# Kernel optimization log

Measured on AMD Instinct MI355X. Metric: run time of the kernel, lower is better.

## Reference

```python
import jax, jax.numpy as jnp
import numpy as np

H = 2048        # hidden_size
NH = 16         # num_heads
NOPE = 128      # qk_nope_head_dim
ROPE = 64       # qk_rope_head_dim
VD = 128        # v_head_dim
QLORA = 1536    # q_lora_rank
KVLORA = 512    # kv_lora_rank
THETA = 1000000.0
EPS = 1e-6
B, S = 2, 2048


def _rope_cos_sin(position_ids):
    # inv_freq over even dims, emb = cat(freqs, freqs); indexed by position_ids
    inv_freq = 1.0 / (THETA ** (jnp.arange(0, ROPE, 2, dtype=jnp.float32) / ROPE))
    freqs = position_ids.astype(jnp.float32)[..., None] * inv_freq  # [b,s,ROPE/2]
    emb = jnp.concatenate([freqs, freqs], axis=-1)                  # [b,s,ROPE]
    # unsqueeze_dim=1 -> broadcast over heads
    return jnp.cos(emb)[:, None], jnp.sin(emb)[:, None]             # [b,1,s,ROPE]


def _apply_rope(x, cos, sin):
    # torch: view(b,h,s,d//2,2).transpose(4,3).reshape -> interleaved-to-half-split permutation
    xp = jnp.concatenate([x[..., 0::2], x[..., 1::2]], axis=-1)
    x1, x2 = jnp.split(xp, 2, axis=-1)
    rot = jnp.concatenate([-x2, x1], axis=-1)  # rotate_half
    return xp * cos + rot * sin


def setup_inputs() -> dict:
    key = jax.random.key(0)
    ks = jax.random.split(key, 7)
    s = 0.02
    hidden_states = jax.random.normal(ks[0], (B, S, H), jnp.float32)
    position_ids = jnp.broadcast_to(jnp.arange(S, dtype=jnp.int64 if jax.config.jax_enable_x64 else jnp.int32), (B, S))
    attention_mask = jnp.broadcast_to(jnp.tril(jnp.ones((S, S), bool))[None, None], (B, 1, S, S))
    Wq_down = jax.random.normal(ks[1], (QLORA, H), jnp.float32) * s
    q_ln_w = jnp.ones((QLORA,), jnp.float32)
    Wq_up = jax.random.normal(ks[2], (NH * (NOPE + ROPE), QLORA), jnp.float32) * s
    Wkv_down = jax.random.normal(ks[3], (KVLORA + ROPE, H), jnp.float32) * s
    Wkv_up = jax.random.normal(ks[4], (NH * (NOPE + VD), KVLORA), jnp.float32) * s
    Wo = jax.random.normal(ks[5], (H, NH * VD), jnp.float32) * s
    return {
        'hidden_states': hidden_states, 'position_ids': position_ids,
        'attention_mask': attention_mask, 'Wq_down': Wq_down, 'q_ln_w': q_ln_w,
        'Wq_up': Wq_up, 'Wkv_down': Wkv_down, 'Wkv_up': Wkv_up, 'Wo': Wo,
    }


def reference(hidden_states, position_ids, attention_mask,
              Wq_down, q_ln_w, Wq_up, Wkv_down, Wkv_up, Wo):
    b, s, _ = hidden_states.shape
    dtype = hidden_states.dtype

    # --- Q path: down-proj -> RMSNorm -> up-proj ---
    ql = hidden_states @ Wq_down.T                                   # [b,s,QLORA]
    var = jnp.mean(jnp.square(ql.astype(jnp.float32)), -1, keepdims=True)
    ql = (q_ln_w * (ql.astype(jnp.float32) * jax.lax.rsqrt(var + EPS)).astype(dtype))
    q = (ql @ Wq_up.T).reshape(b, s, NH, NOPE + ROPE).transpose(0, 2, 1, 3)  # [b,h,s,d]
    q_nope, q_rope = q[..., :NOPE], q[..., NOPE:]

    cos, sin = _rope_cos_sin(position_ids)                           # [b,1,s,ROPE]
    q_rope = _apply_rope(q_rope, cos, sin)                           # [b,h,s,ROPE]

    # --- KV path: single down-proj, split into compressed_kv and rope part ---
    ckv = hidden_states @ Wkv_down.T                                 # [b,s,KVLORA+ROPE]
    compressed_kv, k_rope = ckv[..., :KVLORA], ckv[..., KVLORA:]
    k_rope = _apply_rope(k_rope[:, None], cos, sin)[:, 0]            # [b,s,ROPE]
    # NOTE: kv_down_layernorm is declared in __init__ but never applied in forward.

    # --- absorption trick: fold kv_up into q / output ---
    kv_up = Wkv_up.reshape(NH, NOPE + VD, KVLORA)
    q_absorb = kv_up[:, :NOPE, :]                                    # [h,NOPE,KVLORA]
    out_absorb = kv_up[:, NOPE:, :]                                  # [h,VD,KVLORA]
    q_abs = jnp.einsum('bhsn,hnc->bhsc', q_nope, q_absorb)           # [b,h,s,KVLORA]

    scale = 1.0 / np.sqrt(NOPE + ROPE)
    scores = (jnp.einsum('bhqr,bkr->bhqk', q_rope, k_rope)
              + jnp.einsum('bhqc,bkc->bhqk', q_abs, compressed_kv)) * scale
    scores = jnp.where(attention_mask, scores, -jnp.inf)
    attn = jax.nn.softmax(scores.astype(jnp.float32), axis=-1).astype(dtype)

    out = jnp.einsum('bhqk,bkc->bhqc', attn, compressed_kv)          # [b,h,s,KVLORA]
    out = jnp.einsum('bhqc,hvc->bhqv', out, out_absorb)              # [b,h,s,VD]
    out = out.transpose(0, 2, 1, 3).reshape(b, s, NH * VD)
    return out @ Wo.T                                                # [b,s,H]
```

## Files before the change

kernel.cpp:

```cpp
#include <hip/hip_runtime.h>
#include <cstdint>

#define S_LEN 2048
#define NH_N  16
#define VT_LD 2080

typedef short s16x8 __attribute__((ext_vector_type(8)));
typedef unsigned short u16x8 __attribute__((ext_vector_type(8)));
typedef float f32x4 __attribute__((ext_vector_type(4)));

__device__ __forceinline__ float b2f(unsigned short u) {
    return __uint_as_float(((uint32_t)u) << 16);
}
__device__ __forceinline__ unsigned short f2b(float f) {
    uint32_t x = __float_as_uint(f);
    x += 0x7fffu + ((x >> 16) & 1u);
    return (unsigned short)(x >> 16);
}

__device__ __forceinline__ void cstore(unsigned short* p, float v) { *p = f2b(v); }
__device__ __forceinline__ void cstore(float* p, float v) { *p = v; }

__device__ __forceinline__ void gl2lds16(const void* g, void* l) {
    __builtin_amdgcn_global_load_lds(
        (const __attribute__((address_space(1))) unsigned int*)g,
        (__attribute__((address_space(3))) unsigned int*)l, 16, 0, 0);
}

__device__ __forceinline__ void lds_barrier() {
    asm volatile("s_waitcnt lgkmcnt(0)" ::: "memory");
    __builtin_amdgcn_s_barrier();
    __builtin_amdgcn_sched_barrier(0);
}

__global__ __launch_bounds__(256) void f32_to_bf16(const float* __restrict__ in,
                                                   unsigned short* __restrict__ out,
                                                   long n)
{
    const long nv = n >> 2;
    long i = (long)blockIdx.x * blockDim.x + threadIdx.x;
    const long stride = (long)gridDim.x * blockDim.x;
    for (; i < nv; i += stride) {
        float4 v = ((const float4*)in)[i];
        ushort4 o;
        o.x = f2b(v.x); o.y = f2b(v.y); o.z = f2b(v.z); o.w = f2b(v.w);
        ((ushort4*)out)[i] = o;
    }
}

template <typename CT>
__global__ __launch_bounds__(256) void gemm128(
    const unsigned short* __restrict__ A, const unsigned short* __restrict__ B,
    CT* __restrict__ C,
    int K, int lda, int ldb, int ldc, int Nlim,
    long sAb, long sAh, long sBb, long sBh, long sCb, long sCh)
{
    __shared__ unsigned short Alds[128 * 32];
    __shared__ unsigned short Blds[128 * 32];
    const int z = blockIdx.z, b = z >> 4, h = z & 15;
    A += (long)b * sAb + (long)h * sAh;
    B += (long)b * sBb + (long)h * sBh;
    C += (long)b * sCb + (long)h * sCh;
    const int tid = threadIdx.x;
    const int lane = tid & 63, w = tid >> 6;
    const int l15 = lane & 15, q4 = lane >> 4;
    const int m0 = blockIdx.x * 128, n0 = blockIdx.y * 128;
    const int wm = (w >> 1) * 64, wn = (w & 1) * 64;

    int srow[2], sgc[2];
#pragma unroll
    for (int it = 0; it < 2; ++it) {
        const int g = it * 256 + tid;
        const int row = g >> 2, gp = g & 3;
        srow[it] = row;
        sgc[it] = gp ^ ((row ^ (row >> 2)) & 3);
    }
    int aoff[4], boff[4];
#pragma unroll
    for (int i = 0; i < 4; ++i) {
        const int ra = wm + i * 16 + l15;
        aoff[i] = ra * 32 + (q4 ^ ((ra ^ (ra >> 2)) & 3)) * 8;
        const int rb = wn + i * 16 + l15;
        boff[i] = rb * 32 + (q4 ^ ((rb ^ (rb >> 2)) & 3)) * 8;
    }

    f32x4 acc[4][4];
#pragma unroll
    for (int i = 0; i < 4; ++i)
#pragma unroll
        for (int j = 0; j < 4; ++j) acc[i][j] = (f32x4){0.f, 0.f, 0.f, 0.f};

    for (int k0 = 0; k0 < K; k0 += 32) {
        __syncthreads();
#pragma unroll
        for (int it = 0; it < 2; ++it) {
            gl2lds16(A + (long)(m0 + srow[it]) * lda + k0 + sgc[it] * 8,
                     (char*)Alds + ((it * 256 + w * 64) << 4));
            gl2lds16(B + (long)(n0 + srow[it]) * ldb + k0 + sgc[it] * 8,
                     (char*)Blds + ((it * 256 + w * 64) << 4));
        }
        __syncthreads();
        s16x8 af[4], bf[4];
#pragma unroll
        for (int i = 0; i < 4; ++i) {
            af[i] = *(const s16x8*)(Alds + aoff[i]);
            bf[i] = *(const s16x8*)(Blds + boff[i]);
        }
#pragma unroll
        for (int i = 0; i < 4; ++i)
#pragma unroll
            for (int j = 0; j < 4; ++j)
                acc[i][j] = __builtin_amdgcn_mfma_f32_16x16x32_bf16(af[i], bf[j], acc[i][j], 0, 0, 0);
    }

#pragma unroll
    for (int i = 0; i < 4; ++i) {
        const int row0 = m0 + wm + i * 16 + q4 * 4;
#pragma unroll
        for (int j = 0; j < 4; ++j) {
            const int col = n0 + wn + j * 16 + l15;
            if (col < Nlim) {
#pragma unroll
                for (int r = 0; r < 4; ++r)
                    cstore(&C[(long)(row0 + r) * ldc + col], acc[i][j][r]);
            }
        }
    }
}

__global__ __launch_bounds__(256) void rmsnorm_k(unsigned short* __restrict__ ql,
                                                 const unsigned short* __restrict__ w)
{
    const long base = (long)blockIdx.x * 1536;
    const int tid = threadIdx.x;
    float v[6];
    float ss = 0.f;
#pragma unroll
    for (int i = 0; i < 6; ++i) {
        v[i] = b2f(ql[base + tid + i * 256]);
        ss += v[i] * v[i];
    }
#pragma unroll
    for (int off = 32; off; off >>= 1) ss += __shfl_xor(ss, off, 64);
    __shared__ float red[4];
    if ((tid & 63) == 0) red[tid >> 6] = ss;
    __syncthreads();
    const float tot = red[0] + red[1] + red[2] + red[3];
    const float r = rsqrtf(tot * (1.0f / 1536.0f) + 1e-6f);
#pragma unroll
    for (int i = 0; i < 6; ++i) {
        const int idx = tid + i * 256;
        ql[base + idx] = f2b(v[i] * r * b2f(w[idx]));
    }
}

__global__ __launch_bounds__(512) void rope_k(
    const unsigned short* __restrict__ q, const unsigned short* __restrict__ ckv,
    const int* __restrict__ pos_ids,
    unsigned short* __restrict__ q_rope, unsigned short* __restrict__ krope)
{
    const int bs = blockIdx.x;
    const int b = bs >> 11, s = bs & 2047;
    const int t = threadIdx.x;
    const int j = t & 31, h = t >> 5;
    const float pos = (float)pos_ids[bs];
    const float invf = __expf(-(float)j * 0.4317347f);
    float sn, cs;
    sincosf(pos * invf, &sn, &cs);
    const unsigned short* x = q + (long)bs * 3072 + h * 192 + 128;
    const float x0 = b2f(x[2 * j]), x1 = b2f(x[2 * j + 1]);
    const long ob = ((long)(b * NH_N + h) * S_LEN + s) * 64;
    q_rope[ob + j]      = f2b(x0 * cs - x1 * sn);
    q_rope[ob + 32 + j] = f2b(x1 * cs + x0 * sn);
    if (h == 0) {
        const unsigned short* y = ckv + (long)bs * 576 + 512;
        const float y0 = b2f(y[2 * j]), y1 = b2f(y[2 * j + 1]);
        const long ob2 = (long)bs * 64;
        krope[ob2 + j]      = f2b(y0 * cs - y1 * sn);
        krope[ob2 + 32 + j] = f2b(y1 * cs + y0 * sn);
    }
}

__global__ __launch_bounds__(256) void transpose_qabsorb(
    const unsigned short* __restrict__ Wkv_up, unsigned short* __restrict__ qT)
{
    const int idx = blockIdx.x * 256 + threadIdx.x;
    const int n = idx & 127;
    const int c = (idx >> 7) & 511;
    const int h = idx >> 16;
    qT[idx] = Wkv_up[((long)(h * 256 + n)) * 512 + c];
}

__global__ __launch_bounds__(256) void transpose_ckv(
    const unsigned short* __restrict__ ckv, unsigned short* __restrict__ VT_g)
{
    __shared__ unsigned short t[64][72];
    const int k0 = blockIdx.x * 64, c0 = blockIdx.y * 64, b = blockIdx.z;
    const int tid = threadIdx.x;
#pragma unroll
    for (int it = 0; it < 2; ++it) {
        int idx = tid + it * 256;
        int row = idx >> 3, g = idx & 7;
        *(s16x8*)&t[row][g * 8] =
            *(const s16x8*)(ckv + ((long)(b * S_LEN + k0 + row) * 576 + c0 + g * 8));
    }
    __syncthreads();
#pragma unroll
    for (int it = 0; it < 2; ++it) {
        int idx = tid + it * 256;
        int c = idx >> 3, g = idx & 7;
        u16x8 v;
#pragma unroll
        for (int j = 0; j < 8; ++j) v[j] = t[g * 8 + j][c];
        *(u16x8*)(VT_g + ((long)(b * 512 + c0 + c) * VT_LD + k0 + g * 8)) = v;
    }
}

__global__ __launch_bounds__(512, 1) void flash_mfma(
    const unsigned short* __restrict__ qabs,  const unsigned short* __restrict__ qrope,
    const unsigned short* __restrict__ ckv,   const unsigned short* __restrict__ krope,
    const unsigned short* __restrict__ VT_g,  unsigned short* __restrict__ attn_out)
{
    __shared__ unsigned short K_lds[2][2304 * 8];
    __shared__ unsigned short VT_lds[2][2048 * 8];
    __shared__ unsigned short P_lds[8][16 * 40];
    __shared__ float alpha_lds[8 * 16];
    __shared__ float inv_lds[8 * 16];
    __shared__ int   flag_lds[8];

    const float scale2 = 0.10412195f;
    const float THR    = 11.5416f;
    const int tid = threadIdx.x;
    const int lane = tid & 63, w = tid >> 6;
    const int l15 = lane & 15, q4 = lane >> 4;
    const int bh = blockIdx.x;
    const int b = bh >> 4;

    const unsigned short* ckv_b  = ckv   + (long)b * S_LEN * 576;
    const unsigned short* krop_b = krope + (long)b * S_LEN * 64;
    const unsigned short* vt_b   = VT_g  + (long)b * 512 * VT_LD;

    int koff[4], voff[4];
#pragma unroll
    for (int it = 0; it < 4; ++it) {
        const int idx = it * 512 + tid;
        const int key = ((idx >> 6) & 1) * 16 + (idx & 15);
        const int g   = (idx >> 7) * 4 + ((idx >> 4) & 3);
        koff[it] = key * 576 + g * 8;
        const int c   = (idx >> 6) * 16 + (idx & 15);
        voff[it] = c * VT_LD + ((idx >> 4) & 3) * 8;
    }
    const int hoff = (((tid >> 6) & 1) * 16 + (tid & 15)) * 64 +
                     ((tid >> 7) * 4 + ((tid >> 4) & 3)) * 8;

#pragma unroll 1
    for (int half = 0; half < 2; ++half) {
        const int qt = half ? blockIdx.y : 15 - blockIdx.y;
        const int q0 = qt * 128;

        s16x8 qf[18];
        {
            const unsigned short* qa = qabs + ((long)bh * S_LEN + q0 + w * 16 + l15) * 512 + q4 * 8;
#pragma unroll
            for (int kb = 0; kb < 16; ++kb) qf[kb] = *(const s16x8*)(qa + kb * 32);
            const unsigned short* qr = qrope + ((long)bh * S_LEN + q0 + w * 16 + l15) * 64 + q4 * 8;
            qf[16] = *(const s16x8*)(qr);
            qf[17] = *(const s16x8*)(qr + 32);
        }

        f32x4 O[32];
#pragma unroll
        for (int i = 0; i < 32; ++i) O[i] = (f32x4){0.f, 0.f, 0.f, 0.f};
        float m_i[4] = {-INFINITY, -INFINITY, -INFINITY, -INFINITY};
        float l_i[4] = {0.f, 0.f, 0.f, 0.f};

        const int nkt = 4 * qt + 4;
        unsigned short *Kc = K_lds[0], *Kn = K_lds[1];
        unsigned short *Vc = VT_lds[0], *Vn = VT_lds[1];

        {
#pragma unroll
            for (int it = 0; it < 4; ++it)
                gl2lds16(ckv_b + koff[it], (char*)Kc + ((it * 512 + w * 64) << 4));
            if (tid < 256)
                gl2lds16(krop_b + hoff, (char*)Kc + ((2048 + w * 64) << 4));
#pragma unroll
            for (int it = 0; it < 4; ++it)
                gl2lds16(vt_b + voff[it], (char*)Vc + ((it * 512 + w * 64) << 4));
        }
        __syncthreads();

        for (int kt = 0; kt < nkt; ++kt) {
            const int k0 = kt * 32;

            if (kt + 1 < nkt) {
                const int kn = k0 + 32;
                const unsigned short* cs = ckv_b + (long)kn * 576;
#pragma unroll
                for (int it = 0; it < 4; ++it)
                    gl2lds16(cs + koff[it], (char*)Kn + ((it * 512 + w * 64) << 4));
                if (tid < 256)
                    gl2lds16(krop_b + (long)kn * 64 + hoff, (char*)Kn + ((2048 + w * 64) << 4));
                const unsigned short* vs = vt_b + kn;
#pragma unroll
                for (int it = 0; it < 4; ++it)
                    gl2lds16(vs + voff[it], (char*)Vn + ((it * 512 + w * 64) << 4));
            }

            if (k0 <= q0 + (w << 4) + 15) {
                f32x4 s0 = {0.f, 0.f, 0.f, 0.f}, s1 = s0;
                __builtin_amdgcn_s_setprio(1);
#pragma unroll
                for (int kb = 0; kb < 18; ++kb) {
                    s16x8 k0f = *(const s16x8*)&Kc[((kb * 2 + 0) * 64 + lane) * 8];
                    s16x8 k1f = *(const s16x8*)&Kc[((kb * 2 + 1) * 64 + lane) * 8];
                    s0 = __builtin_amdgcn_mfma_f32_16x16x32_bf16(qf[kb], k0f, s0, 0, 0, 0);
                    s1 = __builtin_amdgcn_mfma_f32_16x16x32_bf16(qf[kb], k1f, s1, 0, 0, 0);
                }
                __builtin_amdgcn_s_setprio(0);
#pragma unroll
                for (int r = 0; r < 4; ++r) { s0[r] *= scale2; s1[r] *= scale2; }
                if (k0 + 31 > q0 + (w << 4)) {
#pragma unroll
                    for (int r = 0; r < 4; ++r) {
                        const int qg = q0 + w * 16 + q4 * 4 + r;
                        if (k0 + l15 > qg)      s0[r] = -INFINITY;
                        if (k0 + 16 + l15 > qg) s1[r] = -INFINITY;
                    }
                }

                float mx[4];
#pragma unroll
                for (int r = 0; r < 4; ++r) {
                    float m = fmaxf(s0[r], s1[r]);
#pragma unroll
                    for (int off = 1; off < 16; off <<= 1) m = fmaxf(m, __shfl_xor(m, off, 64));
                    mx[r] = m;
                }
                bool need = false;
#pragma unroll
                for (int r = 0; r < 4; ++r) need = need || (mx[r] - m_i[r] > THR);
                const bool needw = __any(need);
                float al[4] = {1.f, 1.f, 1.f, 1.f};
                if (needw) {
#pragma unroll
                    for (int r = 0; r < 4; ++r) {
                        const float mn = fmaxf(m_i[r], mx[r]);
                        al[r] = exp2f(m_i[r] - mn);
                        m_i[r] = mn;
                        l_i[r] *= al[r];
                    }
                }
                if (l15 == 0)
                    *(f32x4*)&alpha_lds[w * 16 + q4 * 4] = (f32x4){al[0], al[1], al[2], al[3]};
                if (lane == 0) flag_lds[w] = needw ? 1 : 0;
#pragma unroll
                for (int r = 0; r < 4; ++r) {
                    const float p0 = exp2f(s0[r] - m_i[r]);
                    const float p1 = exp2f(s1[r] - m_i[r]);
                    l_i[r] += p0 + p1;
                    P_lds[w][(q4 * 4 + r) * 40 + l15]      = f2b(p0);
                    P_lds[w][(q4 * 4 + r) * 40 + 16 + l15] = f2b(p1);
                }
            } else {
                if (lane == 0) flag_lds[w] = 0;
            }

            lds_barrier();

            {
                int4 f0 = *(const int4*)&flag_lds[0];
                int4 f1 = *(const int4*)&flag_lds[4];
                if (f0.x | f0.y | f0.z | f0.w | f1.x | f1.y | f1.z | f1.w) {
#pragma unroll
                    for (int rb = 0; rb < 8; ++rb) {
                        if (k0 <= q0 + rb * 16 + 15) {
                            f32x4 alr = *(const f32x4*)&alpha_lds[rb * 16 + q4 * 4];
#pragma unroll
                            for (int cb = 0; cb < 4; ++cb)
#pragma unroll
                                for (int r = 0; r < 4; ++r)
                                    O[rb * 4 + cb][r] *= alr[r];
                        }
                    }
                }
            }

            {
                s16x8 vh[4];
#pragma unroll
                for (int cb = 0; cb < 4; ++cb)
                    vh[cb] = *(const s16x8*)&Vc[((w * 4 + cb) * 64 + lane) * 8];
#pragma unroll
                for (int rb = 0; rb < 8; ++rb) {
                    if (k0 <= q0 + rb * 16 + 15) {
                        s16x8 pa = *(const s16x8*)&P_lds[rb][l15 * 40 + q4 * 8];
                        __builtin_amdgcn_s_setprio(1);
#pragma unroll
                        for (int cb = 0; cb < 4; ++cb)
                            O[rb * 4 + cb] = __builtin_amdgcn_mfma_f32_16x16x32_bf16(pa, vh[cb], O[rb * 4 + cb], 0, 0, 0);
                        __builtin_amdgcn_s_setprio(0);
                    }
                }
            }

            __syncthreads();
            unsigned short* t;
            t = Kc; Kc = Kn; Kn = t;
            t = Vc; Vc = Vn; Vn = t;
        }

#pragma unroll
        for (int r = 0; r < 4; ++r) {
            float ls = l_i[r];
#pragma unroll
            for (int off = 1; off < 16; off <<= 1) ls += __shfl_xor(ls, off, 64);
            l_i[r] = 1.0f / ls;
        }
        if (l15 == 0)
            *(f32x4*)&inv_lds[w * 16 + q4 * 4] = (f32x4){l_i[0], l_i[1], l_i[2], l_i[3]};
        lds_barrier();
#pragma unroll
        for (int rb = 0; rb < 8; ++rb) {
            f32x4 ivr = *(const f32x4*)&inv_lds[rb * 16 + q4 * 4];
#pragma unroll
            for (int r = 0; r < 4; ++r) {
                const long rowbase = ((long)bh * S_LEN + q0 + rb * 16 + q4 * 4 + r) * 512;
#pragma unroll
                for (int cb = 0; cb < 4; ++cb)
                    attn_out[rowbase + w * 64 + cb * 16 + l15] = f2b(O[rb * 4 + cb][r] * ivr[r]);
            }
        }
        __syncthreads();
    }
}

extern "C" void kernel_launch(void* const* d_in, const int* in_sizes, int n_in,
                              void* d_out, int out_size, void* d_ws, size_t ws_size,
                              hipStream_t stream)
{
    (void)in_sizes; (void)n_in; (void)out_size; (void)ws_size;
    const float* hs_f       = (const float*)d_in[0];
    const int*   pos        = (const int*)d_in[1];
    const float* Wq_down_f  = (const float*)d_in[3];
    const float* q_ln_w_f   = (const float*)d_in[4];
    const float* Wq_up_f    = (const float*)d_in[5];
    const float* Wkv_down_f = (const float*)d_in[6];
    const float* Wkv_up_f   = (const float*)d_in[7];
    const float* Wo_f       = (const float*)d_in[8];
    float* out = (float*)d_out;

    unsigned short* ws    = (unsigned short*)d_ws;
    unsigned short* ql    = ws;
    unsigned short* q     = ql    + 4096L * 1536;
    unsigned short* out2  = q;
    unsigned short* ckv   = q     + 4096L * 3072;
    unsigned short* krope = ckv   + 4096L * 576;
    unsigned short* qrope = krope + 4096L * 64;
    unsigned short* qabsT = qrope + 32L * 2048 * 64;
    unsigned short* qabs  = qabsT + 16L * 512 * 128;
    unsigned short* attno = qabs  + 32L * 2048 * 512;
    unsigned short* hs    = attno + 32L * 2048 * 512;
    unsigned short* Wqd   = hs    + 4096L * 2048;
    unsigned short* qlnw  = Wqd   + 1536L * 2048;
    unsigned short* Wqu   = qlnw  + 1536;
    unsigned short* Wkvd  = Wqu   + 3072L * 1536;
    unsigned short* Wkvu  = Wkvd  + 576L * 2048;
    unsigned short* Wob   = Wkvu  + 16L * 256 * 512;
    unsigned short* VTg   = Wob   + 2048L * 2048;

    f32_to_bf16<<<4096, 256, 0, stream>>>(hs_f,       hs,   4096L * 2048);
    f32_to_bf16<<<3072, 256, 0, stream>>>(Wq_down_f,  Wqd,  1536L * 2048);
    f32_to_bf16<<<2,    256, 0, stream>>>(q_ln_w_f,   qlnw, 1536L);
    f32_to_bf16<<<4096, 256, 0, stream>>>(Wq_up_f,    Wqu,  3072L * 1536);
    f32_to_bf16<<<1152, 256, 0, stream>>>(Wkv_down_f, Wkvd, 576L * 2048);
    f32_to_bf16<<<2048, 256, 0, stream>>>(Wkv_up_f,   Wkvu, 16L * 256 * 512);
    f32_to_bf16<<<4096, 256, 0, stream>>>(Wo_f,       Wob,  2048L * 2048);

    gemm128<unsigned short><<<dim3(32, 12, 1), 256, 0, stream>>>(hs, Wqd, ql,
        2048, 2048, 2048, 1536, 1536, 0, 0, 0, 0, 0, 0);
    rmsnorm_k<<<4096, 256, 0, stream>>>(ql, qlnw);
    gemm128<unsigned short><<<dim3(32, 24, 1), 256, 0, stream>>>(ql, Wqu, q,
        1536, 1536, 1536, 3072, 3072, 0, 0, 0, 0, 0, 0);
    gemm128<unsigned short><<<dim3(32, 5, 1), 256, 0, stream>>>(hs, Wkvd, ckv,
        2048, 2048, 2048, 576, 576, 0, 0, 0, 0, 0, 0);
    rope_k<<<4096, 512, 0, stream>>>(q, ckv, pos, qrope, krope);
    transpose_ckv<<<dim3(32, 8, 2), 256, 0, stream>>>(ckv, VTg);
    transpose_qabsorb<<<4096, 256, 0, stream>>>(Wkvu, qabsT);
    gemm128<unsigned short><<<dim3(16, 4, 32), 256, 0, stream>>>(q, qabsT, qabs,
        128, 3072, 128, 512, 512,
        2048L * 3072, 192, 0, 512L * 128, 16L * 2048 * 512, 2048L * 512);
    flash_mfma<<<dim3(32, 8, 1), 512, 0, stream>>>(qabs, qrope, ckv, krope, VTg, attno);
    gemm128<unsigned short><<<dim3(16, 1, 32), 256, 0, stream>>>(attno, Wkvu + 128L * 512, out2,
        512, 512, 512, 2048, 128,
        16L * 2048 * 512, 2048L * 512, 0, 256L * 512, 2048L * 2048, 128);
    gemm128<float><<<dim3(32, 16, 1), 256, 0, stream>>>(out2, Wob, out,
        2048, 2048, 2048, 2048, 2048, 0, 0, 0, 0, 0, 0);
}
```

Baseline: 766.4 us.

## Software-pipeline PV by one tile and single-buffer V to drop mid-loop barrier

The flash attention loop now runs the P·V MFMA for the previous key tile after the current tile's QK and softmax. This removes the intra-iteration LDS barrier between softmax and PV. P, alpha and flag buffers are double-buffered by tile parity. V is single-buffered: each wave reads its V fragments into registers, waits on lgkmcnt, then issues the next V tile load into the same LDS slot. This frees LDS and overlaps the V load with QK, but relies on each wave only touching its own V slice and adds an epilogue PV step.

```diff
diff --git a/kernel.cpp b/kernel.cpp
--- a/kernel.cpp
+++ b/kernel.cpp
@@ -222,11 +222,11 @@
     const unsigned short* __restrict__ VT_g,  unsigned short* __restrict__ attn_out)
 {
     __shared__ unsigned short K_lds[2][2304 * 8];
-    __shared__ unsigned short VT_lds[2][2048 * 8];
-    __shared__ unsigned short P_lds[8][16 * 40];
-    __shared__ float alpha_lds[8 * 16];
-    __shared__ float inv_lds[8 * 16];
-    __shared__ int   flag_lds[8];
+    __shared__ unsigned short V_lds[2048 * 8];
+    __shared__ unsigned short P_lds[2][8][16 * 40];
+    __shared__ __align__(16) float alpha_lds[2][8 * 16];
+    __shared__ __align__(16) float inv_lds[8 * 16];
+    __shared__ int flag_lds[2][8];
 
     const float scale2 = 0.10412195f;
     const float THR    = 11.5416f;
@@ -240,18 +240,21 @@
     const unsigned short* krop_b = krope + (long)b * S_LEN * 64;
     const unsigned short* vt_b   = VT_g  + (long)b * 512 * VT_LD;
 
-    int koff[4], voff[4];
+    int koff[4];
 #pragma unroll
     for (int it = 0; it < 4; ++it) {
         const int idx = it * 512 + tid;
         const int key = ((idx >> 6) & 1) * 16 + (idx & 15);
         const int g   = (idx >> 7) * 4 + ((idx >> 4) & 3);
         koff[it] = key * 576 + g * 8;
-        const int c   = (idx >> 6) * 16 + (idx & 15);
-        voff[it] = c * VT_LD + ((idx >> 4) & 3) * 8;
     }
     const int hoff = (((tid >> 6) & 1) * 16 + (tid & 15)) * 64 +
                      ((tid >> 7) * 4 + ((tid >> 4) & 3)) * 8;
+
+    long vsoff[4];
+#pragma unroll
+    for (int i = 0; i < 4; ++i)
+        vsoff[i] = (long)((w * 4 + i) * 16 + l15) * VT_LD + q4 * 8;
 
 #pragma unroll 1
     for (int half = 0; half < 2; ++half) {
@@ -276,7 +279,6 @@
 
         const int nkt = 4 * qt + 4;
         unsigned short *Kc = K_lds[0], *Kn = K_lds[1];
-        unsigned short *Vc = VT_lds[0], *Vn = VT_lds[1];
 
         {
 #pragma unroll
@@ -284,14 +286,44 @@
                 gl2lds16(ckv_b + koff[it], (char*)Kc + ((it * 512 + w * 64) << 4));
             if (tid < 256)
                 gl2lds16(krop_b + hoff, (char*)Kc + ((2048 + w * 64) << 4));
-#pragma unroll
-            for (int it = 0; it < 4; ++it)
-                gl2lds16(vt_b + voff[it], (char*)Vc + ((it * 512 + w * 64) << 4));
         }
         __syncthreads();
+
+#define PV_TILE(PRV, K0P, VH)                                                              \
+        {                                                                                  \
+            const int* fp = flag_lds[PRV];                                                 \
+            const int anyf = fp[0] | fp[1] | fp[2] | fp[3] | fp[4] | fp[5] | fp[6] | fp[7];\
+            if (anyf) {                                                                    \
+                _Pragma("unroll")                                                          \
+                for (int rb = 0; rb < 8; ++rb) {                                           \
+                    if ((K0P) <= q0 + rb * 16 + 15) {                                      \
+                        f32x4 alr = *(const f32x4*)&alpha_lds[PRV][rb * 16 + q4 * 4];      \
+                        _Pragma("unroll")                                                  \
+                        for (int cb = 0; cb < 4; ++cb)                                     \
+                            _Pragma("unroll")                                              \
+                            for (int r = 0; r < 4; ++r)                                    \
+                                O[rb * 4 + cb][r] *= alr[r];                               \
+                    }                                                                      \
+                }                                                                          \
+            }                                                                              \
+            _Pragma("unroll")                                                              \
+            for (int rb = 0; rb < 8; ++rb) {                                               \
+                if ((K0P) <= q0 + rb * 16 + 15) {                                          \
+                    s16x8 pa = *(const s16x8*)&P_lds[PRV][rb][l15 * 40 + q4 * 8];          \
+                    __builtin_amdgcn_s_setprio(1);                                         \
+                    _Pragma("unroll")                                                      \
+                    for (int cb = 0; cb < 4; ++cb)                                         \
+                        O[rb * 4 + cb] = __builtin_amdgcn_mfma_f32_16x16x32_bf16(          \
+                            pa, VH[cb], O[rb * 4 + cb], 0, 0, 0);                          \
+                    __builtin_amdgcn_s_setprio(0);                                         \
+                }                                                                          \
+            }                                                                              \
+        }
 
         for (int kt = 0; kt < nkt; ++kt) {
             const int k0 = kt * 32;
+            const int cur = kt & 1, prv = cur ^ 1;
+            const int k0p = k0 - 32;
 
             if (kt + 1 < nkt) {
                 const int kn = k0 + 32;
@@ -301,11 +333,18 @@
                     gl2lds16(cs + koff[it], (char*)Kn + ((it * 512 + w * 64) << 4));
                 if (tid < 256)
                     gl2lds16(krop_b + (long)kn * 64 + hoff, (char*)Kn + ((2048 + w * 64) << 4));
-                const unsigned short* vs = vt_b + kn;
-#pragma unroll
-                for (int it = 0; it < 4; ++it)
-                    gl2lds16(vs + voff[it], (char*)Vn + ((it * 512 + w * 64) << 4));
             }
+
+            s16x8 vh[4];
+            if (kt > 0) {
+#pragma unroll
+                for (int cb = 0; cb < 4; ++cb)
+                    vh[cb] = *(const s16x8*)&V_lds[((w * 4 + cb) * 64 + lane) * 8];
+            }
+            asm volatile("s_waitcnt lgkmcnt(0)" ::: "memory");
+#pragma unroll
+            for (int i = 0; i < 4; ++i)
+                gl2lds16(vt_b + vsoff[i] + k0, (char*)V_lds + ((w * 256 + i * 64) << 4));
 
             if (k0 <= q0 + (w << 4) + 15) {
                 f32x4 s0 = {0.f, 0.f, 0.f, 0.f}, s1 = s0;
@@ -352,63 +391,39 @@
                     }
                 }
                 if (l15 == 0)
-                    *(f32x4*)&alpha_lds[w * 16 + q4 * 4] = (f32x4){al[0], al[1], al[2], al[3]};
-                if (lane == 0) flag_lds[w] = needw ? 1 : 0;
+                    *(f32x4*)&alpha_lds[cur][w * 16 + q4 * 4] = (f32x4){al[0], al[1], al[2], al[3]};
+                if (lane == 0) flag_lds[cur][w] = needw ? 1 : 0;
 #pragma unroll
                 for (int r = 0; r < 4; ++r) {
                     const float p0 = exp2f(s0[r] - m_i[r]);
                     const float p1 = exp2f(s1[r] - m_i[r]);
                     l_i[r] += p0 + p1;
-                    P_lds[w][(q4 * 4 + r) * 40 + l15]      = f2b(p0);
-                    P_lds[w][(q4 * 4 + r) * 40 + 16 + l15] = f2b(p1);
+                    P_lds[cur][w][(q4 * 4 + r) * 40 + l15]      = f2b(p0);
+                    P_lds[cur][w][(q4 * 4 + r) * 40 + 16 + l15] = f2b(p1);
                 }
             } else {
-                if (lane == 0) flag_lds[w] = 0;
+                if (lane == 0) flag_lds[cur][w] = 0;
             }
 
-            lds_barrier();
-
-            {
-                int4 f0 = *(const int4*)&flag_lds[0];
-                int4 f1 = *(const int4*)&flag_lds[4];
-                if (f0.x | f0.y | f0.z | f0.w | f1.x | f1.y | f1.z | f1.w) {
-#pragma unroll
-                    for (int rb = 0; rb < 8; ++rb) {
-                        if (k0 <= q0 + rb * 16 + 15) {
-                            f32x4 alr = *(const f32x4*)&alpha_lds[rb * 16 + q4 * 4];
-#pragma unroll
-                            for (int cb = 0; cb < 4; ++cb)
-#pragma unroll
-                                for (int r = 0; r < 4; ++r)
-                                    O[rb * 4 + cb][r] *= alr[r];
-                        }
-                    }
-                }
-            }
-
-            {
-                s16x8 vh[4];
-#pragma unroll
-                for (int cb = 0; cb < 4; ++cb)
-                    vh[cb] = *(const s16x8*)&Vc[((w * 4 + cb) * 64 + lane) * 8];
-#pragma unroll
-                for (int rb = 0; rb < 8; ++rb) {
-                    if (k0 <= q0 + rb * 16 + 15) {
-                        s16x8 pa = *(const s16x8*)&P_lds[rb][l15 * 40 + q4 * 8];
-                        __builtin_amdgcn_s_setprio(1);
-#pragma unroll
-                        for (int cb = 0; cb < 4; ++cb)
-                            O[rb * 4 + cb] = __builtin_amdgcn_mfma_f32_16x16x32_bf16(pa, vh[cb], O[rb * 4 + cb], 0, 0, 0);
-                        __builtin_amdgcn_s_setprio(0);
-                    }
-                }
+            if (kt > 0) {
+                PV_TILE(prv, k0p, vh)
             }
 
             __syncthreads();
             unsigned short* t;
             t = Kc; Kc = Kn; Kn = t;
-            t = Vc; Vc = Vn; Vn = t;
-        }
+        }
+
+        {
+            const int prv = (nkt - 1) & 1;
+            const int k0p = (nkt - 1) * 32;
+            s16x8 vh[4];
+#pragma unroll
+            for (int cb = 0; cb < 4; ++cb)
+                vh[cb] = *(const s16x8*)&V_lds[((w * 4 + cb) * 64 + lane) * 8];
+            PV_TILE(prv, k0p, vh)
+        }
+#undef PV_TILE
 
 #pragma unroll
         for (int r = 0; r < 4; ++r) {
```

After: 839.0 us. +9.5%, slower.
